# Kernel tuning notes

Measured on AMD Instinct MI355X. Metric: run time of the kernel, lower is better.

## Reference

```python
import math
import jax, jax.numpy as jnp
import numpy as np

H = 16          # n_heads
WIN = 512       # window_size (causal, one-sided)
BS = 64         # block_size


def setup_inputs() -> dict:
    key = jax.random.key(0)
    ks = jax.random.split(key, 5)
    B, T, D = 2, 4096, 1024
    x = jax.random.normal(ks[0], (B, T, D), dtype=jnp.float32)
    init = 0.02
    Wq = jax.random.normal(ks[1], (D, D), dtype=jnp.float32) * init
    Wk = jax.random.normal(ks[2], (D, D), dtype=jnp.float32) * init
    Wv = jax.random.normal(ks[3], (D, D), dtype=jnp.float32) * init
    Wo = jax.random.normal(ks[4], (D, D), dtype=jnp.float32) * init
    return {"x": x, "Wq": Wq, "Wk": Wk, "Wv": Wv, "Wo": Wo}


def _sliding_window_attn(q, k, v):
    """Causal sliding-window attention, banded/block-sparse form.

    q,k,v: (B, H, T, hd). Only key blocks within the window of each query
    block are gathered, honoring the sparsity the torch mask encodes.
    """
    B, Hn, T, hd = q.shape
    nb = T // BS                   # number of blocks
    nw1 = WIN // BS + 1            # key blocks touching a query block
    scale = 1.0 / math.sqrt(hd)

    qb = q.reshape(B, Hn, nb, BS, hd)
    kb = k.reshape(B, Hn, nb, BS, hd)
    vb = v.reshape(B, Hn, nb, BS, hd)

    offs = jnp.arange(-(WIN // BS), 1)                 # (nw1,)
    idx_raw = jnp.arange(nb)[:, None] + offs[None, :]  # (nb, nw1)
    idx = jnp.clip(idx_raw, 0, nb - 1)

    kg = jnp.take(kb, idx, axis=2)   # (B,H,nb,nw1,BS,hd)
    vg = jnp.take(vb, idx, axis=2)

    scores = jnp.einsum('bhnqd,bhnwkd->bhnqwk', qb, kg) * scale

    qpos = (jnp.arange(nb) * BS)[:, None, None, None] + jnp.arange(BS)[None, :, None, None]  # (nb,BS,1,1)
    kpos = (idx_raw * BS)[:, None, :, None] + jnp.arange(BS)[None, None, None, :]            # (nb,1,nw1,BS)
    valid = (idx_raw[:, None, :, None] >= 0) & (kpos <= qpos) & (qpos - kpos < WIN)
    scores = jnp.where(valid[None, None], scores, -1e9)

    p = jax.nn.softmax(scores.reshape(B, Hn, nb, BS, nw1 * BS), axis=-1)
    p = p.reshape(B, Hn, nb, BS, nw1, BS)
    out = jnp.einsum('bhnqwk,bhnwkd->bhnqd', p, vg)
    return out.reshape(B, Hn, T, hd)


def reference(x, Wq, Wk, Wv, Wo):
    B, T, D = x.shape
    hd = D // H

    def proj(W):  # torch Linear: x @ W.T
        return (x @ W.T).reshape(B, T, H, hd).transpose(0, 2, 1, 3)

    q, k, v = proj(Wq), proj(Wk), proj(Wv)
    out = _sliding_window_attn(q, k, v)            # (B,H,T,hd)
    out = out.transpose(0, 2, 1, 3).reshape(B, T, D)
    return out @ Wo.T
```

## Files before the change

kernel.cpp:

```cpp
#include <hip/hip_runtime.h>

#define DI static __device__ __forceinline__

typedef __attribute__((ext_vector_type(8))) short short8;
typedef __attribute__((ext_vector_type(4))) float f32x4;

DI unsigned short f2bf(float f) {
    union { float f; unsigned int u; } v; v.f = f;
    unsigned int r = v.u + 0x7FFFu + ((v.u >> 16) & 1u);
    return (unsigned short)(r >> 16);
}

DI void gload_lds16(const void* g, void* l) {
    __builtin_amdgcn_global_load_lds(
        (const __attribute__((address_space(1))) void*)g,
        (__attribute__((address_space(3))) void*)l, 16, 0, 0);
}

DI short8 ldsfrag(const void* base, int row, int bytecol) {
    return *(const short8*)((const char*)base + row * 128 + (bytecol ^ ((row & 7) << 4)));
}

__global__ __launch_bounds__(256) void k_cvt(
    const float* __restrict__ x, const float* __restrict__ wq,
    const float* __restrict__ wk, const float* __restrict__ wv,
    const float* __restrict__ wo,
    unsigned short* __restrict__ xb, unsigned short* __restrict__ wqb,
    unsigned short* __restrict__ wkb, unsigned short* __restrict__ wvb,
    unsigned short* __restrict__ wob)
{
    int idx = (blockIdx.x * 256 + threadIdx.x) * 4;
    const float* src; unsigned short* dst; int off;
    if (idx < 8388608) {
        src = x; dst = xb; off = idx;
    } else {
        int rel = idx - 8388608;
        int sel = rel >> 20;
        off = rel & 1048575;
        switch (sel) {
            case 0:  src = wq; dst = wqb; break;
            case 1:  src = wk; dst = wkb; break;
            case 2:  src = wv; dst = wvb; break;
            default: src = wo; dst = wob; break;
        }
    }
    float4 v = *(const float4*)(src + off);
    unsigned long long o = (unsigned long long)f2bf(v.x)
        | ((unsigned long long)f2bf(v.y) << 16)
        | ((unsigned long long)f2bf(v.z) << 32)
        | ((unsigned long long)f2bf(v.w) << 48);
    *(unsigned long long*)(dst + off) = o;
}

DI void gemm_core(const unsigned short* __restrict__ Ag,
                  const unsigned short* __restrict__ Bg,
                  int m0, int n0, char* smem, f32x4 acc[4][4])
{
    const int t = threadIdx.x, lane = t & 63;
    const int wid = t >> 6, wr = wid >> 2, wc = wid & 3;
    const int kl = lane & 15, hi = lane >> 4;

#pragma unroll
    for (int m = 0; m < 4; ++m)
#pragma unroll
        for (int n = 0; n < 4; ++n)
            acc[m][n] = f32x4{0.f, 0.f, 0.f, 0.f};

    const int ca  = t,       ra  = ca  >> 2, sa  = ((ca  & 3) ^ ((ra  >> 1) & 3)) * 8;
    const int cb0 = t,       rb0 = cb0 >> 2, sb0 = ((cb0 & 3) ^ ((rb0 >> 1) & 3)) * 8;
    const int cb1 = t + 512, rb1 = cb1 >> 2, sb1 = ((cb1 & 3) ^ ((rb1 >> 1) & 3)) * 8;
    const unsigned short* pa  = Ag + (long)(m0 + ra)  * 1024 + sa;
    const unsigned short* pb0 = Bg + (long)(n0 + rb0) * 1024 + sb0;
    const unsigned short* pb1 = Bg + (long)(n0 + rb1) * 1024 + sb1;

#define STAGE(TILE, BUF) do {                                          \
        char* _sb = smem + (BUF) * 24576;                              \
        gload_lds16(pa  + (TILE) * 32, _sb + ca * 16);                 \
        gload_lds16(pb0 + (TILE) * 32, _sb + 8192 + cb0 * 16);         \
        gload_lds16(pb1 + (TILE) * 32, _sb + 8192 + cb1 * 16);         \
    } while (0)

    STAGE(0, 0);
    STAGE(1, 1);

    const int swz = ((hi ^ ((kl >> 1) & 3)) << 4);
    const int aoff = (wr * 64 + kl) * 64 + swz;
    const int boff = 8192 + (wc * 64 + kl) * 64 + swz;

#define KSTEP(KS, CUR, PRE, ISSUE, VM) do {                                   \
        asm volatile("s_waitcnt vmcnt(" VM ")" ::: "memory");                 \
        __builtin_amdgcn_s_barrier();                                         \
        __builtin_amdgcn_sched_barrier(0);                                    \
        if (ISSUE) STAGE((KS) + 2, PRE);                                      \
        const char* _ab = smem + (CUR) * 24576 + aoff;                        \
        const char* _bb = smem + (CUR) * 24576 + boff;                        \
        short8 _fa[4], _fb[4];                                                \
        _Pragma("unroll")                                                     \
        for (int m = 0; m < 4; ++m) _fa[m] = *(const short8*)(_ab + m * 1024);\
        _Pragma("unroll")                                                     \
        for (int n = 0; n < 4; ++n) _fb[n] = *(const short8*)(_bb + n * 1024);\
        __builtin_amdgcn_s_setprio(1);                                        \
        _Pragma("unroll")                                                     \
        for (int m = 0; m < 4; ++m)                                           \
        _Pragma("unroll")                                                     \
            for (int n = 0; n < 4; ++n)                                       \
                acc[m][n] = __builtin_amdgcn_mfma_f32_16x16x32_bf16(          \
                    _fa[m], _fb[n], acc[m][n], 0, 0, 0);                      \
        __builtin_amdgcn_s_setprio(0);                                        \
    } while (0)

    for (int u = 0; u < 10; ++u) {
        const int ks = u * 3;
        KSTEP(ks + 0, 0, 2, 1, "3");
        KSTEP(ks + 1, 1, 0, 1, "3");
        KSTEP(ks + 2, 2, 1, 1, "3");
    }
    KSTEP(30, 0, 2, 0, "3");
    KSTEP(31, 1, 0, 0, "0");
#undef KSTEP
#undef STAGE
}

__global__ __launch_bounds__(512, 4) void k_gemm_qkv(
    const unsigned short* __restrict__ xb,
    const unsigned short* __restrict__ wqb, const unsigned short* __restrict__ wkb,
    const unsigned short* __restrict__ wvb,
    unsigned short* __restrict__ Qo, unsigned short* __restrict__ Ko,
    unsigned short* __restrict__ VTo)
{
    extern __shared__ char smem[];
    const int bx = blockIdx.x, by = blockIdx.y;
    const int w = by >> 2, nb = by & 3;
    const unsigned short* Bw = (w == 0) ? wqb : ((w == 1) ? wkb : wvb);
    const float sc = (w == 0) ? 0.125f : 1.0f;

    f32x4 acc[4][4];
    gemm_core(xb, Bw, bx * 128, nb * 256, smem, acc);

    const int t = threadIdx.x, lane = t & 63, wid = t >> 6;
    const int wr = wid >> 2, wc = wid & 3, kl = lane & 15, hi = lane >> 4;
    const int h = nb * 4 + wc;

    if (w < 2) {
        unsigned short* Ow = (w == 0) ? Qo : Ko;
#pragma unroll
        for (int m = 0; m < 4; ++m)
#pragma unroll
            for (int r = 0; r < 4; ++r) {
                int grow = bx * 128 + wr * 64 + m * 16 + hi * 4 + r;
                int bi = grow >> 12, tt = grow & 4095;
                unsigned short* rowp = Ow + ((long)(bi * 16 + h) * 4096 + tt) * 64;
#pragma unroll
                for (int n = 0; n < 4; ++n)
                    rowp[n * 16 + kl] = f2bf(acc[m][n][r] * sc);
            }
    } else {
#pragma unroll
        for (int m = 0; m < 4; ++m)
#pragma unroll
            for (int r = 0; r < 4; ++r) {
                int grow = bx * 128 + wr * 64 + m * 16 + hi * 4 + r;
                int bi = grow >> 12, tt = grow & 4095;
                unsigned short* hb = VTo + (long)(bi * 16 + h) * 262144;
#pragma unroll
                for (int n = 0; n < 4; ++n) {
                    int d = n * 16 + kl;
                    hb[(long)d * 4096 + tt] = f2bf(acc[m][n][r]);
                }
            }
    }
}

__global__ __launch_bounds__(256) void k_attn(
    const unsigned short* __restrict__ Q, const unsigned short* __restrict__ K,
    const unsigned short* __restrict__ VT, unsigned short* __restrict__ AO)
{
    __shared__ unsigned short Qs[4096];
    __shared__ unsigned short Ks[2][4096], Vs[2][4096];
    const int t = threadIdx.x, lane = t & 63, wid = t >> 6;
    const int kl = lane & 15, hi = lane >> 4;
    const int bid = blockIdx.x;
    const int sid = (bid & 7) * 256 + (bid >> 3);
    const int i = sid & 63, bh = sid >> 6;
    const int b = bh >> 4, h = bh & 15;
    const char* qg = (const char*)(Q + ((long)bh * 4096 + i * 64) * 64);
    const char* kg = (const char*)(K + (long)bh * 4096 * 64);
    const char* vg = (const char*)(VT + (long)bh * 64 * 4096);

    const int c0 = t, c1 = t + 256;
    const int r0 = c0 >> 3, sw0 = ((c0 & 7) * 16) ^ ((r0 & 7) << 4);
    const int r1 = c1 >> 3, sw1 = ((c1 & 7) * 16) ^ ((r1 & 7) << 4);
    const char* kg0 = kg + r0 * 128 + sw0;
    const char* kg1 = kg + r1 * 128 + sw1;
    const char* vg0 = vg + r0 * 8192 + sw0;
    const char* vg1 = vg + r1 * 8192 + sw1;

    const int j0 = (i >= 8) ? i - 8 : 0;

    gload_lds16(qg + r0 * 128 + sw0, (char*)Qs + c0 * 16);
    gload_lds16(qg + r1 * 128 + sw1, (char*)Qs + c1 * 16);
    gload_lds16(kg0 + j0 * 8192, (char*)Ks[0] + c0 * 16);
    gload_lds16(kg1 + j0 * 8192, (char*)Ks[0] + c1 * 16);
    gload_lds16(vg0 + j0 * 128,  (char*)Vs[0] + c0 * 16);
    gload_lds16(vg1 + j0 * 128,  (char*)Vs[0] + c1 * 16);
    __syncthreads();

    short8 aq[2];
    aq[0] = ldsfrag(Qs, wid * 16 + kl, hi * 16);
    aq[1] = ldsfrag(Qs, wid * 16 + kl, 64 + hi * 16);

    float lsum[4] = {0.f, 0.f, 0.f, 0.f};
    f32x4 o[4];
#pragma unroll
    for (int nt = 0; nt < 4; ++nt) o[nt] = f32x4{0.f, 0.f, 0.f, 0.f};

    const int qrow = wid * 16 + hi * 4;
    char* pw = (char*)Qs + wid * 2048;

    for (int j = j0; j <= i; ++j) {
        const int buf = (j - j0) & 1;
        if (j < i) {
            const int nb = buf ^ 1;
            gload_lds16(kg0 + (j + 1) * 8192, (char*)Ks[nb] + c0 * 16);
            gload_lds16(kg1 + (j + 1) * 8192, (char*)Ks[nb] + c1 * 16);
            gload_lds16(vg0 + (j + 1) * 128,  (char*)Vs[nb] + c0 * 16);
            gload_lds16(vg1 + (j + 1) * 128,  (char*)Vs[nb] + c1 * 16);
        }

        f32x4 s[4];
#pragma unroll
        for (int nt = 0; nt < 4; ++nt) {
            s[nt] = f32x4{0.f, 0.f, 0.f, 0.f};
#pragma unroll
            for (int kk = 0; kk < 2; ++kk)
                s[nt] = __builtin_amdgcn_mfma_f32_16x16x32_bf16(
                    aq[kk], ldsfrag(Ks[buf], nt * 16 + kl, kk * 64 + hi * 16),
                    s[nt], 0, 0, 0);
        }

        if (j == i) {
#pragma unroll
            for (int nt = 0; nt < 4; ++nt) {
                int key = nt * 16 + kl;
#pragma unroll
                for (int r = 0; r < 4; ++r)
                    if (key > qrow + r) s[nt][r] = -1e9f;
            }
        } else if (i - j == 8) {
#pragma unroll
            for (int nt = 0; nt < 4; ++nt) {
                int key = nt * 16 + kl;
#pragma unroll
                for (int r = 0; r < 4; ++r)
                    if (key <= qrow + r) s[nt][r] = -1e9f;
            }
        }

#pragma unroll
        for (int nt = 0; nt < 4; ++nt)
#pragma unroll
            for (int r = 0; r < 4; ++r) {
                float p = __expf(s[nt][r]);
                s[nt][r] = p;
                lsum[r] += p;
            }

#pragma unroll
        for (int nt = 0; nt < 4; ++nt)
#pragma unroll
            for (int r = 0; r < 4; ++r) {
                int q = hi * 4 + r;
                int colb = (nt * 16 + kl) * 2;
                *(unsigned short*)(pw + q * 128 + (colb ^ ((q & 7) << 4))) =
                    f2bf(s[nt][r]);
            }

        short8 pa0 = ldsfrag(pw, kl, hi * 16);
        short8 pa1 = ldsfrag(pw, kl, 64 + hi * 16);
#pragma unroll
        for (int nt = 0; nt < 4; ++nt) {
            o[nt] = __builtin_amdgcn_mfma_f32_16x16x32_bf16(
                pa0, ldsfrag(Vs[buf], nt * 16 + kl, hi * 16), o[nt], 0, 0, 0);
            o[nt] = __builtin_amdgcn_mfma_f32_16x16x32_bf16(
                pa1, ldsfrag(Vs[buf], nt * 16 + kl, 64 + hi * 16), o[nt], 0, 0, 0);
        }

        __syncthreads();
    }

#pragma unroll
    for (int d = 1; d < 16; d <<= 1)
#pragma unroll
        for (int r = 0; r < 4; ++r) lsum[r] += __shfl_xor(lsum[r], d);

    float inv[4];
#pragma unroll
    for (int r = 0; r < 4; ++r) inv[r] = 1.0f / lsum[r];
#pragma unroll
    for (int r = 0; r < 4; ++r) {
        int tt = i * 64 + wid * 16 + hi * 4 + r;
        unsigned short* rowp = AO + ((long)(b * 4096 + tt)) * 1024 + h * 64;
#pragma unroll
        for (int nt = 0; nt < 4; ++nt)
            rowp[nt * 16 + kl] = f2bf(o[nt][r] * inv[r]);
    }
}

__global__ __launch_bounds__(512, 4) void k_gemm_out(
    const unsigned short* __restrict__ AO, const unsigned short* __restrict__ wob,
    float* __restrict__ out)
{
    extern __shared__ char smem[];
    const int bx = blockIdx.x, nb = blockIdx.y;
    f32x4 acc[4][4];
    gemm_core(AO, wob, bx * 128, nb * 256, smem, acc);

    const int t = threadIdx.x, lane = t & 63, wid = t >> 6;
    const int wr = wid >> 2, wc = wid & 3, kl = lane & 15, hi = lane >> 4;
#pragma unroll
    for (int m = 0; m < 4; ++m)
#pragma unroll
        for (int r = 0; r < 4; ++r) {
            int grow = bx * 128 + wr * 64 + m * 16 + hi * 4 + r;
            float* rowp = out + (long)grow * 1024 + nb * 256 + wc * 64;
#pragma unroll
            for (int n = 0; n < 4; ++n)
                rowp[n * 16 + kl] = acc[m][n][r];
        }
}

extern "C" void kernel_launch(void* const* d_in, const int* in_sizes, int n_in,
                              void* d_out, int out_size, void* d_ws, size_t ws_size,
                              hipStream_t stream) {
    const float* x  = (const float*)d_in[0];
    const float* wq = (const float*)d_in[1];
    const float* wk = (const float*)d_in[2];
    const float* wv = (const float*)d_in[3];
    const float* wo = (const float*)d_in[4];

    char* ws = (char*)d_ws;
    const size_t MB = 1024 * 1024;
    unsigned short* xb  = (unsigned short*)(ws);
    unsigned short* wqb = (unsigned short*)(ws + 16 * MB);
    unsigned short* wkb = (unsigned short*)(ws + 18 * MB);
    unsigned short* wvb = (unsigned short*)(ws + 20 * MB);
    unsigned short* wob = (unsigned short*)(ws + 22 * MB);
    unsigned short* Qp  = (unsigned short*)(ws + 24 * MB);
    unsigned short* Kp  = (unsigned short*)(ws + 40 * MB);
    unsigned short* VTp = (unsigned short*)(ws + 56 * MB);
    unsigned short* AOp = xb;

    hipFuncSetAttribute((const void*)k_gemm_qkv,
                        hipFuncAttributeMaxDynamicSharedMemorySize, 73728);
    hipFuncSetAttribute((const void*)k_gemm_out,
                        hipFuncAttributeMaxDynamicSharedMemorySize, 73728);

    dim3 blk(256);
    k_cvt<<<12288, blk, 0, stream>>>(x, wq, wk, wv, wo,
                                     xb, wqb, wkb, wvb, wob);
    k_gemm_qkv<<<dim3(64, 12), 512, 73728, stream>>>(xb, wqb, wkb, wvb,
                                                     Qp, Kp, VTp);
    k_attn<<<2048, blk, 0, stream>>>(Qp, Kp, VTp, AOp);
    k_gemm_out<<<dim3(64, 4), 512, 73728, stream>>>(AOp, wob, (float*)d_out);
}
```

Before: 138.4 us.

## Share K/V tiles across two query blocks, use exp2 softmax, retile output GEMM

The attention kernel now runs 512-thread blocks that each handle two adjacent query blocks, so every K/V tile loaded into LDS serves both. Each half of the waves skips key blocks outside its own window. Q is pre-scaled by log2(e)/8 so the softmax can use exp2f instead of __expf. The output projection GEMM moves to a 128x128 tile with 256 threads and smaller LDS, which doubles its grid to raise occupancy. In exchange, some waves sit idle at the edges of the shared key range, and the attention kernel has half as many blocks.

```diff
diff --git a/kernel.cpp b/kernel.cpp
--- a/kernel.cpp
+++ b/kernel.cpp
@@ -121,6 +121,76 @@
 #undef STAGE
 }
 
+DI void gemm_core128(const unsigned short* __restrict__ Ag,
+                     const unsigned short* __restrict__ Bg,
+                     int m0, int n0, char* smem, f32x4 acc[4][4])
+{
+    const int t = threadIdx.x, lane = t & 63;
+    const int wid = t >> 6, wr = wid >> 1, wc = wid & 1;
+    const int kl = lane & 15, hi = lane >> 4;
+
+#pragma unroll
+    for (int m = 0; m < 4; ++m)
+#pragma unroll
+        for (int n = 0; n < 4; ++n)
+            acc[m][n] = f32x4{0.f, 0.f, 0.f, 0.f};
+
+    const int ca0 = t,       ra0 = ca0 >> 2, sa0 = ((ca0 & 3) ^ ((ra0 >> 1) & 3)) * 8;
+    const int ca1 = t + 256, ra1 = ca1 >> 2, sa1 = ((ca1 & 3) ^ ((ra1 >> 1) & 3)) * 8;
+    const unsigned short* pa0 = Ag + (long)(m0 + ra0) * 1024 + sa0;
+    const unsigned short* pa1 = Ag + (long)(m0 + ra1) * 1024 + sa1;
+    const unsigned short* pb0 = Bg + (long)(n0 + ra0) * 1024 + sa0;
+    const unsigned short* pb1 = Bg + (long)(n0 + ra1) * 1024 + sa1;
+
+#define STAGE(TILE, BUF) do {                                          \
+        char* _sb = smem + (BUF) * 16384;                              \
+        gload_lds16(pa0 + (TILE) * 32, _sb + ca0 * 16);                \
+        gload_lds16(pa1 + (TILE) * 32, _sb + ca1 * 16);                \
+        gload_lds16(pb0 + (TILE) * 32, _sb + 8192 + ca0 * 16);         \
+        gload_lds16(pb1 + (TILE) * 32, _sb + 8192 + ca1 * 16);         \
+    } while (0)
+
+    STAGE(0, 0);
+    STAGE(1, 1);
+
+    const int swz = ((hi ^ ((kl >> 1) & 3)) << 4);
+    const int aoff = (wr * 64 + kl) * 64 + swz;
+    const int boff = 8192 + (wc * 64 + kl) * 64 + swz;
+
+#define KSTEP(KS, CUR, PRE, ISSUE, VM) do {                                   \
+        asm volatile("s_waitcnt vmcnt(" VM ")" ::: "memory");                 \
+        __builtin_amdgcn_s_barrier();                                         \
+        __builtin_amdgcn_sched_barrier(0);                                    \
+        if (ISSUE) STAGE((KS) + 2, PRE);                                      \
+        const char* _ab = smem + (CUR) * 16384 + aoff;                        \
+        const char* _bb = smem + (CUR) * 16384 + boff;                        \
+        short8 _fa[4], _fb[4];                                                \
+        _Pragma("unroll")                                                     \
+        for (int m = 0; m < 4; ++m) _fa[m] = *(const short8*)(_ab + m * 1024);\
+        _Pragma("unroll")                                                     \
+        for (int n = 0; n < 4; ++n) _fb[n] = *(const short8*)(_bb + n * 1024);\
+        __builtin_amdgcn_s_setprio(1);                                        \
+        _Pragma("unroll")                                                     \
+        for (int m = 0; m < 4; ++m)                                           \
+        _Pragma("unroll")                                                     \
+            for (int n = 0; n < 4; ++n)                                       \
+                acc[m][n] = __builtin_amdgcn_mfma_f32_16x16x32_bf16(          \
+                    _fa[m], _fb[n], acc[m][n], 0, 0, 0);                      \
+        __builtin_amdgcn_s_setprio(0);                                        \
+    } while (0)
+
+    for (int u = 0; u < 10; ++u) {
+        const int ks = u * 3;
+        KSTEP(ks + 0, 0, 2, 1, "4");
+        KSTEP(ks + 1, 1, 0, 1, "4");
+        KSTEP(ks + 2, 2, 1, 1, "4");
+    }
+    KSTEP(30, 0, 2, 0, "4");
+    KSTEP(31, 1, 0, 0, "0");
+#undef KSTEP
+#undef STAGE
+}
+
 __global__ __launch_bounds__(512, 4) void k_gemm_qkv(
     const unsigned short* __restrict__ xb,
     const unsigned short* __restrict__ wqb, const unsigned short* __restrict__ wkb,
@@ -132,7 +202,7 @@
     const int bx = blockIdx.x, by = blockIdx.y;
     const int w = by >> 2, nb = by & 3;
     const unsigned short* Bw = (w == 0) ? wqb : ((w == 1) ? wkb : wvb);
-    const float sc = (w == 0) ? 0.125f : 1.0f;
+    const float sc = (w == 0) ? 0.18033688011112042f : 1.0f;
 
     f32x4 acc[4][4];
     gemm_core(xb, Bw, bx * 128, nb * 256, smem, acc);
@@ -171,38 +241,38 @@
     }
 }
 
-__global__ __launch_bounds__(256) void k_attn(
+__global__ __launch_bounds__(512) void k_attn(
     const unsigned short* __restrict__ Q, const unsigned short* __restrict__ K,
     const unsigned short* __restrict__ VT, unsigned short* __restrict__ AO)
 {
-    __shared__ unsigned short Qs[4096];
+    __shared__ unsigned short Qs[8192];
     __shared__ unsigned short Ks[2][4096], Vs[2][4096];
     const int t = threadIdx.x, lane = t & 63, wid = t >> 6;
     const int kl = lane & 15, hi = lane >> 4;
     const int bid = blockIdx.x;
-    const int sid = (bid & 7) * 256 + (bid >> 3);
-    const int i = sid & 63, bh = sid >> 6;
+    const int sid = (bid & 7) * 128 + (bid >> 3);
+    const int qi = sid & 31, bh = sid >> 5;
     const int b = bh >> 4, h = bh & 15;
-    const char* qg = (const char*)(Q + ((long)bh * 4096 + i * 64) * 64);
+    const int iA = qi * 2, iB = qi * 2 + 1;
+    const int myI = (wid < 4) ? iA : iB;
+    const char* qg = (const char*)(Q + ((long)bh * 4096 + qi * 128) * 64);
     const char* kg = (const char*)(K + (long)bh * 4096 * 64);
     const char* vg = (const char*)(VT + (long)bh * 64 * 4096);
 
-    const int c0 = t, c1 = t + 256;
-    const int r0 = c0 >> 3, sw0 = ((c0 & 7) * 16) ^ ((r0 & 7) << 4);
-    const int r1 = c1 >> 3, sw1 = ((c1 & 7) * 16) ^ ((r1 & 7) << 4);
-    const char* kg0 = kg + r0 * 128 + sw0;
-    const char* kg1 = kg + r1 * 128 + sw1;
-    const char* vg0 = vg + r0 * 8192 + sw0;
-    const char* vg1 = vg + r1 * 8192 + sw1;
-
-    const int j0 = (i >= 8) ? i - 8 : 0;
-
-    gload_lds16(qg + r0 * 128 + sw0, (char*)Qs + c0 * 16);
-    gload_lds16(qg + r1 * 128 + sw1, (char*)Qs + c1 * 16);
-    gload_lds16(kg0 + j0 * 8192, (char*)Ks[0] + c0 * 16);
-    gload_lds16(kg1 + j0 * 8192, (char*)Ks[0] + c1 * 16);
-    gload_lds16(vg0 + j0 * 128,  (char*)Vs[0] + c0 * 16);
-    gload_lds16(vg1 + j0 * 128,  (char*)Vs[0] + c1 * 16);
+    const int cq0 = t, cq1 = t + 512;
+    const int rq0 = cq0 >> 3, sq0 = ((cq0 & 7) * 16) ^ ((rq0 & 7) << 4);
+    const int rq1 = cq1 >> 3, sq1 = ((cq1 & 7) * 16) ^ ((rq1 & 7) << 4);
+    const int rk = t >> 3, swk = ((t & 7) * 16) ^ ((rk & 7) << 4);
+    const char* kgt = kg + rk * 128 + swk;
+    const char* vgt = vg + rk * 8192 + swk;
+
+    const int jlo = (iA >= 8) ? iA - 8 : 0;
+    const int jhi = iB;
+
+    gload_lds16(qg + rq0 * 128 + sq0, (char*)Qs + cq0 * 16);
+    gload_lds16(qg + rq1 * 128 + sq1, (char*)Qs + cq1 * 16);
+    gload_lds16(kgt + jlo * 8192, (char*)Ks[0] + t * 16);
+    gload_lds16(vgt + jlo * 128,  (char*)Vs[0] + t * 16);
     __syncthreads();
 
     short8 aq[2];
@@ -214,77 +284,78 @@
 #pragma unroll
     for (int nt = 0; nt < 4; ++nt) o[nt] = f32x4{0.f, 0.f, 0.f, 0.f};
 
-    const int qrow = wid * 16 + hi * 4;
+    const int qrow = (wid & 3) * 16 + hi * 4;
     char* pw = (char*)Qs + wid * 2048;
 
-    for (int j = j0; j <= i; ++j) {
-        const int buf = (j - j0) & 1;
-        if (j < i) {
+    for (int j = jlo; j <= jhi; ++j) {
+        const int buf = (j - jlo) & 1;
+        if (j < jhi) {
             const int nb = buf ^ 1;
-            gload_lds16(kg0 + (j + 1) * 8192, (char*)Ks[nb] + c0 * 16);
-            gload_lds16(kg1 + (j + 1) * 8192, (char*)Ks[nb] + c1 * 16);
-            gload_lds16(vg0 + (j + 1) * 128,  (char*)Vs[nb] + c0 * 16);
-            gload_lds16(vg1 + (j + 1) * 128,  (char*)Vs[nb] + c1 * 16);
+            gload_lds16(kgt + (j + 1) * 8192, (char*)Ks[nb] + t * 16);
+            gload_lds16(vgt + (j + 1) * 128,  (char*)Vs[nb] + t * 16);
         }
 
-        f32x4 s[4];
-#pragma unroll
-        for (int nt = 0; nt < 4; ++nt) {
-            s[nt] = f32x4{0.f, 0.f, 0.f, 0.f};
-#pragma unroll
-            for (int kk = 0; kk < 2; ++kk)
-                s[nt] = __builtin_amdgcn_mfma_f32_16x16x32_bf16(
-                    aq[kk], ldsfrag(Ks[buf], nt * 16 + kl, kk * 64 + hi * 16),
-                    s[nt], 0, 0, 0);
-        }
-
-        if (j == i) {
+        const bool act = (wid < 4) ? (j <= iA) : (j >= iB - 8);
+        if (act) {
+            f32x4 s[4];
 #pragma unroll
             for (int nt = 0; nt < 4; ++nt) {
-                int key = nt * 16 + kl;
-#pragma unroll
-                for (int r = 0; r < 4; ++r)
-                    if (key > qrow + r) s[nt][r] = -1e9f;
+                s[nt] = f32x4{0.f, 0.f, 0.f, 0.f};
+#pragma unroll
+                for (int kk = 0; kk < 2; ++kk)
+                    s[nt] = __builtin_amdgcn_mfma_f32_16x16x32_bf16(
+                        aq[kk], ldsfrag(Ks[buf], nt * 16 + kl, kk * 64 + hi * 16),
+                        s[nt], 0, 0, 0);
             }
-        } else if (i - j == 8) {
+
+            if (j == myI) {
+#pragma unroll
+                for (int nt = 0; nt < 4; ++nt) {
+                    int key = nt * 16 + kl;
+#pragma unroll
+                    for (int r = 0; r < 4; ++r)
+                        if (key > qrow + r) s[nt][r] = -1e9f;
+                }
+            } else if (myI - j == 8) {
+#pragma unroll
+                for (int nt = 0; nt < 4; ++nt) {
+                    int key = nt * 16 + kl;
+#pragma unroll
+                    for (int r = 0; r < 4; ++r)
+                        if (key <= qrow + r) s[nt][r] = -1e9f;
+                }
+            }
+
+#pragma unroll
+            for (int nt = 0; nt < 4; ++nt)
+#pragma unroll
+                for (int r = 0; r < 4; ++r) {
+                    float p = exp2f(s[nt][r]);
+                    s[nt][r] = p;
+                    lsum[r] += p;
+                }
+
+#pragma unroll
+            for (int nt = 0; nt < 4; ++nt)
+#pragma unroll
+                for (int r = 0; r < 4; ++r) {
+                    int q = hi * 4 + r;
+                    int colb = (nt * 16 + kl) * 2;
+                    *(unsigned short*)(pw + q * 128 + (colb ^ ((q & 7) << 4))) =
+                        f2bf(s[nt][r]);
+                }
+
+            short8 pa0 = ldsfrag(pw, kl, hi * 16);
+            short8 pa1 = ldsfrag(pw, kl, 64 + hi * 16);
 #pragma unroll
             for (int nt = 0; nt < 4; ++nt) {
-                int key = nt * 16 + kl;
-#pragma unroll
-                for (int r = 0; r < 4; ++r)
-                    if (key <= qrow + r) s[nt][r] = -1e9f;
+                o[nt] = __builtin_amdgcn_mfma_f32_16x16x32_bf16(
+                    pa0, ldsfrag(Vs[buf], nt * 16 + kl, hi * 16), o[nt], 0, 0, 0);
+                o[nt] = __builtin_amdgcn_mfma_f32_16x16x32_bf16(
+                    pa1, ldsfrag(Vs[buf], nt * 16 + kl, 64 + hi * 16), o[nt], 0, 0, 0);
             }
         }
 
-#pragma unroll
-        for (int nt = 0; nt < 4; ++nt)
-#pragma unroll
-            for (int r = 0; r < 4; ++r) {
-                float p = __expf(s[nt][r]);
-                s[nt][r] = p;
-                lsum[r] += p;
-            }
-
-#pragma unroll
-        for (int nt = 0; nt < 4; ++nt)
-#pragma unroll
-            for (int r = 0; r < 4; ++r) {
-                int q = hi * 4 + r;
-                int colb = (nt * 16 + kl) * 2;
-                *(unsigned short*)(pw + q * 128 + (colb ^ ((q & 7) << 4))) =
-                    f2bf(s[nt][r]);
-            }
-
-        short8 pa0 = ldsfrag(pw, kl, hi * 16);
-        short8 pa1 = ldsfrag(pw, kl, 64 + hi * 16);
-#pragma unroll
-        for (int nt = 0; nt < 4; ++nt) {
-            o[nt] = __builtin_amdgcn_mfma_f32_16x16x32_bf16(
-                pa0, ldsfrag(Vs[buf], nt * 16 + kl, hi * 16), o[nt], 0, 0, 0);
-            o[nt] = __builtin_amdgcn_mfma_f32_16x16x32_bf16(
-                pa1, ldsfrag(Vs[buf], nt * 16 + kl, 64 + hi * 16), o[nt], 0, 0, 0);
-        }
-
         __syncthreads();
     }
 
@@ -298,7 +369,7 @@
     for (int r = 0; r < 4; ++r) inv[r] = 1.0f / lsum[r];
 #pragma unroll
     for (int r = 0; r < 4; ++r) {
-        int tt = i * 64 + wid * 16 + hi * 4 + r;
+        int tt = qi * 128 + wid * 16 + hi * 4 + r;
         unsigned short* rowp = AO + ((long)(b * 4096 + tt)) * 1024 + h * 64;
 #pragma unroll
         for (int nt = 0; nt < 4; ++nt)
@@ -306,23 +377,23 @@
     }
 }
 
-__global__ __launch_bounds__(512, 4) void k_gemm_out(
+__global__ __launch_bounds__(256, 3) void k_gemm_out(
     const unsigned short* __restrict__ AO, const unsigned short* __restrict__ wob,
     float* __restrict__ out)
 {
     extern __shared__ char smem[];
     const int bx = blockIdx.x, nb = blockIdx.y;
     f32x4 acc[4][4];
-    gemm_core(AO, wob, bx * 128, nb * 256, smem, acc);
+    gemm_core128(AO, wob, bx * 128, nb * 128, smem, acc);
 
     const int t = threadIdx.x, lane = t & 63, wid = t >> 6;
-    const int wr = wid >> 2, wc = wid & 3, kl = lane & 15, hi = lane >> 4;
+    const int wr = wid >> 1, wc = wid & 1, kl = lane & 15, hi = lane >> 4;
 #pragma unroll
     for (int m = 0; m < 4; ++m)
 #pragma unroll
         for (int r = 0; r < 4; ++r) {
             int grow = bx * 128 + wr * 64 + m * 16 + hi * 4 + r;
-            float* rowp = out + (long)grow * 1024 + nb * 256 + wc * 64;
+            float* rowp = out + (long)grow * 1024 + nb * 128 + wc * 64;
 #pragma unroll
             for (int n = 0; n < 4; ++n)
                 rowp[n * 16 + kl] = acc[m][n][r];
@@ -353,13 +424,13 @@
     hipFuncSetAttribute((const void*)k_gemm_qkv,
                         hipFuncAttributeMaxDynamicSharedMemorySize, 73728);
     hipFuncSetAttribute((const void*)k_gemm_out,
-                        hipFuncAttributeMaxDynamicSharedMemorySize, 73728);
+                        hipFuncAttributeMaxDynamicSharedMemorySize, 49152);
 
     dim3 blk(256);
     k_cvt<<<12288, blk, 0, stream>>>(x, wq, wk, wv, wo,
                                      xb, wqb, wkb, wvb, wob);
     k_gemm_qkv<<<dim3(64, 12), 512, 73728, stream>>>(xb, wqb, wkb, wvb,
                                                      Qp, Kp, VTp);
-    k_attn<<<2048, blk, 0, stream>>>(Qp, Kp, VTp, AOp);
-    k_gemm_out<<<dim3(64, 4), 512, 73728, stream>>>(AOp, wob, (float*)d_out);
-}
+    k_attn<<<1024, 512, 0, stream>>>(Qp, Kp, VTp, AOp);
+    k_gemm_out<<<dim3(64, 8), 256, 49152, stream>>>(AOp, wob, (float*)d_out);
+}
```

Measured after the change: 136.5 us. About the same (-1.4%).
